# Kernel optimization log

Measured on AMD Instinct MI355X. Metric: run time of the kernel, lower is better.

## Reference

```python
import jax, jax.numpy as jnp
import numpy as np


def conv2d(x, w, b=None):
    # 3x3, stride 1, pad 1, NCHW/OIHW
    y = jax.lax.conv_general_dilated(x, w, (1, 1), ((1, 1), (1, 1)),
                                     dimension_numbers=('NCHW', 'OIHW', 'NCHW'))
    return y if b is None else y + b[None, :, None, None]


def maxpool3s2(x):
    # MaxPool2d(kernel_size=3, stride=2, padding=1)
    return jax.lax.reduce_window(x, -jnp.inf, jax.lax.max,
                                 (1, 1, 3, 3), (1, 1, 2, 2),
                                 ((0, 0), (0, 0), (1, 1), (1, 1)))


def up2(x):
    # F.interpolate(scale_factor=2, mode='bilinear', align_corners=False)
    N, C, H, W = x.shape
    return jax.image.resize(x, (N, C, 2 * H, 2 * W), method='bilinear')


def deform_conv2d(x, offset, w, dg):
    # mmcv-style DeformConv2d (no modulation, no bias), 3x3, pad 1, stride 1.
    # offset: (N, dg*2*9, H, W) -> (N, dg, 9, (y,x), H, W)
    N, Cin, H, W = x.shape
    Cout = w.shape[0]
    K, pad = 9, 1
    Cg = Cin // dg
    off = offset.reshape(N, dg, K, 2, H, W)
    ky, kx = jnp.meshgrid(jnp.arange(3), jnp.arange(3), indexing='ij')
    kdy = (ky.reshape(K) - pad).astype(x.dtype)
    kdx = (kx.reshape(K) - pad).astype(x.dtype)
    gy = jnp.arange(H, dtype=x.dtype)
    gx = jnp.arange(W, dtype=x.dtype)
    py = off[:, :, :, 0] + gy[None, None, None, :, None] + kdy[None, None, :, None, None]
    px = off[:, :, :, 1] + gx[None, None, None, None, :] + kdx[None, None, :, None, None]
    y0f = jnp.floor(py)
    x0f = jnp.floor(px)
    wy = (py - y0f).reshape(N, dg, 1, K * H * W)
    wx = (px - x0f).reshape(N, dg, 1, K * H * W)
    y0 = y0f.astype(jnp.int32)
    x0 = x0f.astype(jnp.int32)
    xg = x.reshape(N, dg, Cg, H * W)

    def gather(yi, xi):
        valid = ((yi >= 0) & (yi < H) & (xi >= 0) & (xi < W))
        idx = (jnp.clip(yi, 0, H - 1) * W + jnp.clip(xi, 0, W - 1)).reshape(N, dg, 1, K * H * W)
        v = jnp.take_along_axis(xg, idx, axis=-1)  # (N, dg, Cg, K*H*W)
        return v * valid.reshape(N, dg, 1, K * H * W).astype(x.dtype)

    v00 = gather(y0, x0)
    v01 = gather(y0, x0 + 1)
    v10 = gather(y0 + 1, x0)
    v11 = gather(y0 + 1, x0 + 1)
    col = (v00 * (1 - wy) * (1 - wx) + v01 * (1 - wy) * wx
           + v10 * wy * (1 - wx) + v11 * wy * wx)
    col = col.reshape(N, Cin, K, H, W)  # im2col with bilinear sampling
    return jnp.einsum('ock,nckhw->nohw', w.reshape(Cout, Cin, K), col)


def pyramid(img, blocks):
    feats = []
    x = img
    for w1, b1, w2, b2 in blocks:
        x = jax.nn.relu(conv2d(x, w1, b1))
        x = jax.nn.relu(conv2d(x, w2, b2))
        x = maxpool3s2(x)
        feats.append(x)
    return feats


def _forward(ref_image, unreg_image,
             fe0_w1, fe0_b1, fe0_w2, fe0_b2,
             fe1_w1, fe1_b1, fe1_w2, fe1_b2,
             fe2_w1, fe2_b1, fe2_w2, fe2_b2,
             ob0_w, ob0_b, ob1_w, ob1_b, ob2_w, ob2_b,
             og0_w, og0_b, og1_w, og1_b, og2_w, og2_b,
             dc0_w, dc1_w, dc2_w,
             fc0_w, fc0_b, fc1_w, fc1_b, fc2_w, fc2_b,
             dob_w, dob_b, dog_w, dog_b, ddc_w):
    relu = jax.nn.relu
    blocks = [(fe0_w1, fe0_b1, fe0_w2, fe0_b2),
              (fe1_w1, fe1_b1, fe1_w2, fe1_b2),
              (fe2_w1, fe2_b1, fe2_w2, fe2_b2)]
    rf = pyramid(ref_image, blocks)
    uf = pyramid(unreg_image, blocks)
    ob = [(ob0_w, ob0_b), (ob1_w, ob1_b), (ob2_w, ob2_b)]
    og = [(og0_w, og0_b), (og1_w, og1_b), (og2_w, og2_b)]
    dc = [dc0_w, dc1_w, dc2_w]
    fc = [(fc0_w, fc0_b), (fc1_w, fc1_b), (fc2_w, fc2_b)]
    offs = [None] * 3
    feats = [None] * 3
    for i in range(2, -1, -1):  # coarse to fine
        o = relu(conv2d(jnp.concatenate([rf[i], uf[i]], axis=1), *ob[i]))
        inp = o if i == 2 else jnp.concatenate([o, up2(offs[i + 1])], axis=1)
        offs[i] = relu(conv2d(inp, *og[i]))  # 18-channel offsets
        f = relu(deform_conv2d(uf[i], offs[i], dc[i], 1))
        finp = f if i == 2 else jnp.concatenate([f, up2(feats[i + 1])], axis=1)
        feats[i] = relu(conv2d(finp, *fc[i]))
    do = conv2d(jnp.concatenate([rf[0], feats[0]], axis=1), dob_w, dob_b)
    do = conv2d(jnp.concatenate([do, offs[0]], axis=1), dog_w, dog_b)  # 36-ch offsets
    return deform_conv2d(feats[0], do, ddc_w, 2)  # (N, 2, H/2, W/2)


def setup_inputs() -> dict:
    key = jax.random.key(0)
    ks = iter(jax.random.split(key, 48))
    IC = 16

    def W(cout, cin):
        return jax.random.normal(next(ks), (cout, cin, 3, 3), jnp.float32) / np.sqrt(cin * 9.0)

    def B(c):
        return jax.random.normal(next(ks), (c,), jnp.float32) * 0.01

    d = {
        'ref_image': jax.random.normal(next(ks), (4, 1, 512, 512), jnp.float32),
        'unreg_image': jax.random.normal(next(ks), (4, 1, 512, 512), jnp.float32),
        'fe0_w1': W(IC, 1), 'fe0_b1': B(IC), 'fe0_w2': W(IC, IC), 'fe0_b2': B(IC),
        'fe1_w1': W(IC, IC), 'fe1_b1': B(IC), 'fe1_w2': W(IC, IC), 'fe1_b2': B(IC),
        'fe2_w1': W(IC, IC), 'fe2_b1': B(IC), 'fe2_w2': W(IC, IC), 'fe2_b2': B(IC),
        'ob0_w': W(IC, 2 * IC), 'ob0_b': B(IC),
        'ob1_w': W(IC, 2 * IC), 'ob1_b': B(IC),
        'ob2_w': W(IC, 2 * IC), 'ob2_b': B(IC),
        'og0_w': W(18, IC + 18), 'og0_b': B(18),
        'og1_w': W(18, IC + 18), 'og1_b': B(18),
        'og2_w': W(18, IC), 'og2_b': B(18),
        'dc0_w': W(IC, IC), 'dc1_w': W(IC, IC), 'dc2_w': W(IC, IC),
        'fc0_w': W(IC, 2 * IC), 'fc0_b': B(IC),
        'fc1_w': W(IC, 2 * IC), 'fc1_b': B(IC),
        'fc2_w': W(IC, IC), 'fc2_b': B(IC),
        'dob_w': W(IC, 2 * IC), 'dob_b': B(IC),
        'dog_w': W(36, IC + 18), 'dog_b': B(36),
        'ddc_w': W(2, IC),
    }
    return d


def reference(ref_image, unreg_image,
              fe0_w1, fe0_b1, fe0_w2, fe0_b2,
              fe1_w1, fe1_b1, fe1_w2, fe1_b2,
              fe2_w1, fe2_b1, fe2_w2, fe2_b2,
              ob0_w, ob0_b, ob1_w, ob1_b, ob2_w, ob2_b,
              og0_w, og0_b, og1_w, og1_b, og2_w, og2_b,
              dc0_w, dc1_w, dc2_w,
              fc0_w, fc0_b, fc1_w, fc1_b, fc2_w, fc2_b,
              dob_w, dob_b, dog_w, dog_b, ddc_w):
    return _forward(ref_image, unreg_image,
                    fe0_w1, fe0_b1, fe0_w2, fe0_b2,
                    fe1_w1, fe1_b1, fe1_w2, fe1_b2,
                    fe2_w1, fe2_b1, fe2_w2, fe2_b2,
                    ob0_w, ob0_b, ob1_w, ob1_b, ob2_w, ob2_b,
                    og0_w, og0_b, og1_w, og1_b, og2_w, og2_b,
                    dc0_w, dc1_w, dc2_w,
                    fc0_w, fc0_b, fc1_w, fc1_b, fc2_w, fc2_b,
                    dob_w, dob_b, dog_w, dog_b, ddc_w)
```

## Files before the change

### kernel.cpp

```cpp
#include <hip/hip_runtime.h>
#include <math.h>

typedef _Float16 half2_t __attribute__((ext_vector_type(2)));
typedef _Float16 half8 __attribute__((ext_vector_type(8)));
typedef float floatx4 __attribute__((ext_vector_type(4)));

__device__ __forceinline__ unsigned packh2(float a, float b) {
  half2_t h;
  h.x = (_Float16)a;
  h.y = (_Float16)b;
  return __builtin_bit_cast(unsigned, h);
}
__device__ __forceinline__ unsigned short f2h(float a) {
  return __builtin_bit_cast(unsigned short, (_Float16)a);
}
__device__ __forceinline__ float h2f(unsigned short u) {
  return (float)__builtin_bit_cast(_Float16, u);
}

__global__ __launch_bounds__(256) void wreorder_k(
    const float* __restrict__ a, const float* __restrict__ b,
    const float* __restrict__ c, const float* __restrict__ d,
    float* __restrict__ out) {
  int t = blockIdx.x * 256 + threadIdx.x;
  if (t < 6912) {
    int which = t / 2304, r = t % 2304;
    int o = r % 16, kc = r / 16;
    int ci = kc % 16, k = kc / 16;
    const float* w = which == 0 ? a : (which == 1 ? b : c);
    out[t] = w[(o * 16 + ci) * 9 + k];
  } else if (t < 7200) {
    int r = t - 6912;
    int o = r % 2, kc = r / 2;
    int ci = kc % 16, k = kc / 16;
    out[t] = d[(o * 16 + ci) * 9 + k];
  }
}

__global__ __launch_bounds__(256) void wmfma_k(
    const float* __restrict__ w0, const float* __restrict__ w1,
    const float* __restrict__ w2, const float* __restrict__ w3,
    const float* __restrict__ w4, const float* __restrict__ w5,
    unsigned short* __restrict__ out) {
  int t = blockIdx.x * 256 + threadIdx.x;
  if (t >= 15360) return;
  int conv = t / 2560, r = t % 2560;
  int c = r / 512, L = (r / 8) % 64, j = r & 7;
  int quad = L >> 4, o = L & 15;
  int k = 32 * c + quad * 8 + j;
  int tap = k >> 4, cin = k & 15;
  float v;
  if (conv == 5) {
    v = (tap < 9 && cin == 0) ? w5[o * 9 + tap] : 0.f;
  } else {
    const float* w = conv == 0 ? w0 : conv == 1 ? w1 : conv == 2 ? w2 : conv == 3 ? w3 : w4;
    v = (tap < 9) ? w[((size_t)o * 16 + cin) * 9 + tap] : 0.f;
  }
  out[t] = f2h(v);
}

struct W32Entry { const float* src; int cin; };
struct W32Table { W32Entry e[8]; };
__global__ __launch_bounds__(256) void wmfma32_k(W32Table t, unsigned short* __restrict__ out) {
  int i = blockIdx.x * 256 + threadIdx.x;
  if (i >= 7 * 4608) return;
  int conv = i / 4608, r = i % 4608;
  int tap = r / 512, L = (r / 8) % 64, j = r & 7;
  int quad = L >> 4, o = L & 15;
  int c = quad * 8 + j;
  W32Entry en = t.e[conv];
  float v = (c < en.cin) ? en.src[((size_t)o * en.cin + c) * 9 + tap] : 0.f;
  out[i] = f2h(v);
}

struct SPEntry { const float* src; int cin; int cout; int ct; int dstoff; };
struct SPTable { SPEntry e[4]; };
__global__ __launch_bounds__(256) void wsplit_k(SPTable t, unsigned short* __restrict__ out) {
  SPEntry en = t.e[blockIdx.y];
  int aSize = en.ct * 2560;
  int bSize = (en.cin > 16) ? en.ct * 4608 : 0;
  int i = blockIdx.x * 256 + threadIdx.x;
  if (i >= aSize + bSize) return;
  float v;
  if (i < aSize) {
    int ct = i / 2560, r = i % 2560;
    int c = r / 512, L = (r / 8) % 64, j = r & 7;
    int quad = L >> 4, o16 = L & 15;
    int k = 32 * c + quad * 8 + j;
    int tap = k >> 4, cin = k & 15;
    int o = ct * 16 + o16;
    v = (tap < 9 && o < en.cout) ? en.src[((size_t)o * en.cin + cin) * 9 + tap] : 0.f;
  } else {
    int r2 = i - aSize;
    int ct = r2 / 4608, r = r2 % 4608;
    int tap = r / 512, L = (r / 8) % 64, j = r & 7;
    int quad = L >> 4, o16 = L & 15;
    int cin = quad * 8 + j;
    int o = ct * 16 + o16;
    v = (cin < en.cin - 16 && o < en.cout)
            ? en.src[((size_t)o * en.cin + 16 + cin) * 9 + tap] : 0.f;
  }
  out[en.dstoff + i] = f2h(v);
}

__device__ __forceinline__ void conv_mfma(
    const unsigned short* __restrict__ src, int SW,
    unsigned short* __restrict__ dst, int DPS, const half8* __restrict__ bf,
    const float* __restrict__ bias, int POS, int OW, int tid, int relu,
    int domask, int gby, int gbx, int bound) {
  const int lane = tid & 63, wid = tid >> 6;
  const int quad = lane >> 4, m = lane & 15;
  const int tap01 = quad >> 1, cin8 = (quad & 1) * 8;
  const int ntiles = (POS + 15) >> 4;
  float bs = bias[m];
  half8 zero;
#pragma unroll
  for (int j = 0; j < 8; ++j) zero[j] = (_Float16)0;
  for (int T = wid; T < ntiles; T += 4) {
    int pa = T * 16 + m;
    pa = pa < POS ? pa : POS - 1;
    int ya = pa / OW, xa = pa - ya * OW;
    floatx4 acc = {0.f, 0.f, 0.f, 0.f};
#pragma unroll
    for (int c = 0; c < 5; ++c) {
      int tap = 2 * c + tap01;
      half8 a = zero;
      if (tap < 9) {
        int dy = tap / 3, dx = tap - (tap / 3) * 3;
        a = *(const half8*)(src + ((ya + dy) * SW + xa + dx) * 16 + cin8);
      }
      acc = __builtin_amdgcn_mfma_f32_16x16x32_f16(a, bf[c], acc, 0, 0, 0);
    }
#pragma unroll
    for (int r = 0; r < 4; ++r) {
      int pd = T * 16 + quad * 4 + r;
      if (pd < POS) {
        float v = acc[r] + bs;
        if (relu) v = fmaxf(v, 0.f);
        if (domask) {
          int yd = pd / OW, xd = pd - (pd / OW) * OW;
          int gy = gby + yd, gx = gbx + xd;
          if (gy < 0 || gy >= bound || gx < 0 || gx >= bound) v = 0.f;
        }
        dst[pd * DPS + m] = f2h(v);
      }
    }
  }
}

__device__ __forceinline__ void conv_mfma32(
    const unsigned short* __restrict__ src, int SW,
    unsigned short* __restrict__ dst, int DPS, const half8* __restrict__ bf,
    const float* __restrict__ bias, int POS, int OW, int tid, int relu,
    int domask, int gby, int gbx, int bound) {
  const int lane = tid & 63, wid = tid >> 6;
  const int quad = lane >> 4, m = lane & 15;
  const int ntiles = (POS + 15) >> 4;
  float bs = bias[m];
  for (int T = wid; T < ntiles; T += 4) {
    int pa = T * 16 + m;
    pa = pa < POS ? pa : POS - 1;
    int ya = pa / OW, xa = pa - ya * OW;
    floatx4 acc = {0.f, 0.f, 0.f, 0.f};
#pragma unroll
    for (int tap = 0; tap < 9; ++tap) {
      int dy = tap / 3, dx = tap - (tap / 3) * 3;
      half8 a = *(const half8*)(src + ((ya + dy) * SW + xa + dx) * 32 + quad * 8);
      acc = __builtin_amdgcn_mfma_f32_16x16x32_f16(a, bf[tap], acc, 0, 0, 0);
    }
#pragma unroll
    for (int r = 0; r < 4; ++r) {
      int pd = T * 16 + quad * 4 + r;
      if (pd < POS) {
        float v = acc[r] + bs;
        if (relu) v = fmaxf(v, 0.f);
        if (domask) {
          int yd = pd / OW, xd = pd - (pd / OW) * OW;
          int gy = gby + yd, gx = gbx + xd;
          if (gy < 0 || gy >= bound || gx < 0 || gx >= bound) v = 0.f;
        }
        dst[pd * DPS + m] = f2h(v);
      }
    }
  }
}

template <int CT, int HASB, int NT>
__device__ __forceinline__ void conv_split_mfma(
    const unsigned short* __restrict__ srcB, const unsigned short* __restrict__ srcO,
    const unsigned short* __restrict__ wbase, float* __restrict__ outLds, int OSTRIDE,
    const float* __restrict__ bias, int NOUT, int relu, int tid) {
  const int lane = tid & 63, wid = tid >> 6;
  const int quad = lane >> 4, m = lane & 15;
  const int tap01 = quad >> 1, cin8 = (quad & 1) * 8;
  half8 zero;
#pragma unroll
  for (int j = 0; j < 8; ++j) zero[j] = (_Float16)0;
  floatx4 acc[CT][NT];
#pragma unroll
  for (int ct = 0; ct < CT; ++ct)
#pragma unroll
    for (int t = 0; t < NT; ++t) acc[ct][t] = floatx4{0.f, 0.f, 0.f, 0.f};
#pragma unroll
  for (int ct = 0; ct < CT; ++ct) {
    half8 bfA[5];
#pragma unroll
    for (int c = 0; c < 5; ++c)
      bfA[c] = *(const half8*)(wbase + ((ct * 5 + c) * 64 + lane) * 8);
#pragma unroll
    for (int t = 0; t < NT; ++t) {
      int pa = (wid + 4 * t) * 16 + m;
      int ya = pa >> 4, xa = pa & 15;
#pragma unroll
      for (int c = 0; c < 5; ++c) {
        int tap = 2 * c + tap01;
        half8 a = zero;
        if (tap < 9) {
          int dy = tap / 3, dx = tap - (tap / 3) * 3;
          a = *(const half8*)(srcB + ((ya + dy) * 18 + xa + dx) * 18 + cin8);
        }
        acc[ct][t] = __builtin_amdgcn_mfma_f32_16x16x32_f16(a, bfA[c], acc[ct][t], 0, 0, 0);
      }
    }
  }
  if (HASB) {
    const unsigned short* wb = wbase + CT * 2560;
#pragma unroll
    for (int ct = 0; ct < CT; ++ct) {
      half8 bfB[9];
#pragma unroll
      for (int c = 0; c < 9; ++c)
        bfB[c] = *(const half8*)(wb + ((ct * 9 + c) * 64 + lane) * 8);
#pragma unroll
      for (int t = 0; t < NT; ++t) {
        int pa = (wid + 4 * t) * 16 + m;
        int ya = pa >> 4, xa = pa & 15;
#pragma unroll
        for (int tap = 0; tap < 9; ++tap) {
          int dy = tap / 3, dx = tap - (tap / 3) * 3;
          half8 a = *(const half8*)(srcO + ((ya + dy) * 18 + xa + dx) * 34 + quad * 8);
          acc[ct][t] = __builtin_amdgcn_mfma_f32_16x16x32_f16(a, bfB[tap], acc[ct][t], 0, 0, 0);
        }
      }
    }
  }
  __syncthreads();
#pragma unroll
  for (int ct = 0; ct < CT; ++ct) {
    int o = ct * 16 + m;
#pragma unroll
    for (int t = 0; t < NT; ++t) {
#pragma unroll
      for (int r = 0; r < 4; ++r) {
        int pd = (wid + 4 * t) * 16 + quad * 4 + r;
        if (o < NOUT) {
          float v = acc[ct][t][r] + bias[o];
          if (relu) v = fmaxf(v, 0.f);
          outLds[pd * OSTRIDE + o] = v;
        }
      }
    }
  }
}

__global__ __launch_bounds__(256) void fe0_fused_k(
    const float* __restrict__ refI, const float* __restrict__ unrI,
    const unsigned short* __restrict__ wm1, const float* __restrict__ b1,
    const unsigned short* __restrict__ wm2, const float* __restrict__ b2,
    float* __restrict__ outR, float* __restrict__ outU, float* __restrict__ outUH) {
  __shared__ __attribute__((aligned(16))) unsigned short bufA[441 * 16];
  __shared__ __attribute__((aligned(16))) unsigned short c1h[361 * 16];
  const int z = blockIdx.z;
  const int im = z >> 2, n = z & 3;
  const float* img = (im ? unrI : refI) + (size_t)n * 512 * 512;
  float* outp = (im ? outU : outR) + (size_t)n * 16 * 256 * 256;
  const int py0 = blockIdx.y * 8, px0 = blockIdx.x * 8;
  const int tid = threadIdx.x;

  half8 bf1[5], bf2[5];
  {
    const int lane = tid & 63;
#pragma unroll
    for (int c = 0; c < 5; ++c) {
      bf1[c] = *(const half8*)(wm1 + (c * 64 + lane) * 8);
      bf2[c] = *(const half8*)(wm2 + (c * 64 + lane) * 8);
    }
  }

  {
    unsigned* s32 = (unsigned*)bufA;
    for (int i = tid; i < 441; i += 256) {
      int yi = i / 21, xi = i - yi * 21;
      int gy = 2 * py0 - 3 + yi, gx = 2 * px0 - 3 + xi;
      float v = 0.f;
      if (gy >= 0 && gy < 512 && gx >= 0 && gx < 512) v = img[gy * 512 + gx];
      uint4 q0 = {packh2(v, 0.f), 0u, 0u, 0u};
      uint4 q1 = {0u, 0u, 0u, 0u};
      *(uint4*)(s32 + i * 8) = q0;
      *(uint4*)(s32 + i * 8 + 4) = q1;
    }
  }
  __syncthreads();

  conv_mfma(bufA, 21, c1h, 16, bf1, b1, 361, 19, tid, 1, 1, 2 * py0 - 2, 2 * px0 - 2, 512);
  __syncthreads();
  conv_mfma(c1h, 19, bufA, 18, bf2, b2, 289, 17, tid, 1, 0, 0, 0, 0);
  __syncthreads();

  unsigned short* stage = c1h;
  for (int i = tid; i < 1024; i += 256) {
    int c = i & 15, r = i >> 4;
    int py = r >> 3, px = r & 7;
    unsigned short m = 0;
#pragma unroll
    for (int dy = 0; dy < 3; ++dy) {
      int gy = 2 * (py0 + py) - 1 + dy;
      if (gy < 0 || gy >= 512) continue;
#pragma unroll
      for (int dx = 0; dx < 3; ++dx) {
        int gx = 2 * (px0 + px) - 1 + dx;
        if (gx < 0 || gx >= 512) continue;
        unsigned short v = bufA[((2 * py + dy) * 17 + 2 * px + dx) * 18 + c];
        m = (v > m) ? v : m;
      }
    }
    stage[r * 18 + c] = m;
  }
  __syncthreads();

  for (int i = tid; i < 1024; i += 256) {
    int c = i >> 6, r = i & 63, py = r >> 3, px = r & 7;
    float mf = h2f(stage[r * 18 + c]);
    outp[((size_t)c * 256 + py0 + py) * 256 + px0 + px] = mf;
    if (im)
      outUH[(((size_t)n * 256 + py0 + py) * 256 + px0 + px) * 16 + c] = mf;
  }
}

__global__ __launch_bounds__(256) void fe12_fused_k(
    const float* __restrict__ in,
    const unsigned short* __restrict__ wm1, const float* __restrict__ b1,
    const unsigned short* __restrict__ wm2, const float* __restrict__ b2,
    float* __restrict__ outC, float* __restrict__ outHWC, int Hin) {
  __shared__ __attribute__((aligned(16))) unsigned short inh[441 * 16];
  __shared__ __attribute__((aligned(16))) unsigned short c1h[361 * 16];
  const int n = blockIdx.z;
  const int Ho = Hin >> 1;
  const int py0 = blockIdx.y * 8, px0 = blockIdx.x * 8;
  const int tid = threadIdx.x;
  const float* inN = in + (size_t)n * 16 * Hin * Hin;
  const size_t HH = (size_t)Hin * Hin;

  half8 bf1[5], bf2[5];
  {
    const int lane = tid & 63;
#pragma unroll
    for (int c = 0; c < 5; ++c) {
      bf1[c] = *(const half8*)(wm1 + (c * 64 + lane) * 8);
      bf2[c] = *(const half8*)(wm2 + (c * 64 + lane) * 8);
    }
  }

  unsigned* inh32 = (unsigned*)inh;
  for (int i = tid; i < 8 * 441; i += 256) {
    int cp = i / 441, r = i - cp * 441;
    int yi = r / 21, xi = r - yi * 21;
    int gy = 2 * py0 - 3 + yi, gx = 2 * px0 - 3 + xi;
    float v0 = 0.f, v1 = 0.f;
    if (gy >= 0 && gy < Hin && gx >= 0 && gx < Hin) {
      const float* s = inN + (size_t)(2 * cp) * HH + (size_t)gy * Hin + gx;
      v0 = s[0];
      v1 = s[HH];
    }
    inh32[r * 8 + cp] = packh2(v0, v1);
  }
  __syncthreads();

  conv_mfma(inh, 21, c1h, 16, bf1, b1, 361, 19, tid, 1, 1, 2 * py0 - 2, 2 * px0 - 2, Hin);
  __syncthreads();
  conv_mfma(c1h, 19, inh, 18, bf2, b2, 289, 17, tid, 1, 0, 0, 0, 0);
  __syncthreads();

  unsigned short* stage = c1h;
  for (int i = tid; i < 1024; i += 256) {
    int c = i & 15, r = i >> 4;
    int py = r >> 3, px = r & 7;
    unsigned short m = 0;
#pragma unroll
    for (int dy = 0; dy < 3; ++dy) {
      int gy = 2 * (py0 + py) - 1 + dy;
      if (gy < 0 || gy >= Hin) continue;
#pragma unroll
      for (int dx = 0; dx < 3; ++dx) {
        int gx = 2 * (px0 + px) - 1 + dx;
        if (gx < 0 || gx >= Hin) continue;
        unsigned short v = inh[((2 * py + dy) * 17 + 2 * px + dx) * 18 + c];
        m = (v > m) ? v : m;
      }
    }
    stage[r * 18 + c] = m;
  }
  __syncthreads();

  float* outp = outC + (size_t)n * 16 * Ho * Ho;
  for (int i = tid; i < 1024; i += 256) {
    int c = i >> 6, r = i & 63, py = r >> 3, px = r & 7;
    float mf = h2f(stage[r * 18 + c]);
    outp[((size_t)c * Ho + py0 + py) * Ho + px0 + px] = mf;
    if (n >= 4)
      outHWC[(((size_t)(n - 4) * Ho + py0 + py) * Ho + px0 + px) * 16 + c] = mf;
  }
}

template <int HAS_UP>
__global__ __launch_bounds__(256) void obog_k(
    const float* __restrict__ rf, const float* __restrict__ uf,
    const float* __restrict__ offsUp,
    const unsigned short* __restrict__ wmob, const float* __restrict__ bob,
    const unsigned short* __restrict__ wog, const float* __restrict__ bog,
    float* __restrict__ offsOut, int H) {
  __shared__ __attribute__((aligned(16))) unsigned POOL[5460];
  const int n = blockIdx.z;
  const int bx = blockIdx.x * 16, by = blockIdx.y * 8;
  const int tid = threadIdx.x;
  const size_t HH = (size_t)H * H;
  const float* r0 = rf + (size_t)n * 16 * HH;
  const float* u0 = uf + (size_t)n * 16 * HH;

  for (int i = tid; i < 3840; i += 256) {
    int cp = i / 240, r = i - cp * 240;
    int ly = r / 20, lx = r - ly * 20;
    int gy = by + ly - 2, gx = bx + lx - 2;
    float v0 = 0.f, v1 = 0.f;
    if (gy >= 0 && gy < H && gx >= 0 && gx < H) {
      const float* s = (cp < 8) ? r0 + (size_t)(2 * cp) * HH : u0 + (size_t)(2 * cp - 16) * HH;
      size_t off = (size_t)gy * H + gx;
      v0 = s[off];
      v1 = s[HH + off];
    }
    POOL[r * 16 + cp] = packh2(v0, v1);
  }
  __syncthreads();

  {
    half8 bf[9];
    const int lane = tid & 63;
#pragma unroll
    for (int c = 0; c < 9; ++c) bf[c] = *(const half8*)(wmob + (c * 64 + lane) * 8);
    conv_mfma32((const unsigned short*)POOL, 20, (unsigned short*)(POOL + 3840), 18,
                bf, bob, 180, 18, tid, 1, 1, by - 1, bx - 1, H);
  }
  __syncthreads();

  if (HAS_UP) {
    const int H2 = H >> 1;
    const float* os = offsUp + (size_t)n * 18 * H2 * H2;
    for (int i = tid; i < 16 * 180; i += 256) {
      int cp = i / 180, r = i - cp * 180;
      unsigned val = 0u;
      if (cp < 9) {
        int y1 = r / 18, x1 = r - y1 * 18;
        int gy = by + y1 - 1, gx = bx + x1 - 1;
        if (gy >= 0 && gy < H && gx >= 0 && gx < H) {
          float sy = 0.5f * gy - 0.25f, sx = 0.5f * gx - 0.25f;
          float y0f = floorf(sy), x0f = floorf(sx);
          float wy = sy - y0f, wx = sx - x0f;
          int y0 = (int)y0f, x0 = (int)x0f;
          int y0c = min(max(y0, 0), H2 - 1), y1c = min(max(y0 + 1, 0), H2 - 1);
          int x0c = min(max(x0, 0), H2 - 1), x1c = min(max(x0 + 1, 0), H2 - 1);
          const float* sp = os + (size_t)(2 * cp) * H2 * H2;
          float v0 = (1.f - wy) * ((1.f - wx) * sp[y0c * H2 + x0c] + wx * sp[y0c * H2 + x1c]) +
                     wy * ((1.f - wx) * sp[y1c * H2 + x0c] + wx * sp[y1c * H2 + x1c]);
          sp += (size_t)H2 * H2;
          float v1 = (1.f - wy) * ((1.f - wx) * sp[y0c * H2 + x0c] + wx * sp[y0c * H2 + x1c]) +
                     wy * ((1.f - wx) * sp[y1c * H2 + x0c] + wx * sp[y1c * H2 + x1c]);
          val = packh2(v0, v1);
        }
      }
      POOL[r * 17 + cp] = val;
    }
    __syncthreads();
  }

  conv_split_mfma<2, HAS_UP, 2>((const unsigned short*)(POOL + 3840),
                                (const unsigned short*)POOL, wog,
                                (float*)POOL, 19, bog, 18, 1, tid);
  __syncthreads();

  {
    int pix = tid & 127, half = tid >> 7;
    const float* of = (const float*)POOL + (size_t)pix * 19 + half * 9;
    int ty = pix >> 4, tx = pix & 15;
    float* op = offsOut + (size_t)n * 18 * HH + (size_t)(half * 9) * HH +
                (size_t)(by + ty) * H + (bx + tx);
#pragma unroll
    for (int o = 0; o < 9; ++o) op[(size_t)o * HH] = of[o];
  }
}

template <int HAS_UP>
__global__ __launch_bounds__(256) void defc_k(
    const float* __restrict__ ufHWC, const float* __restrict__ offs,
    const float* __restrict__ wdef, const float* __restrict__ featsUp,
    const unsigned short* __restrict__ wmfc, const float* __restrict__ bfc,
    float* __restrict__ featsOut, float* __restrict__ outHwc, int H) {
  __shared__ __attribute__((aligned(16))) unsigned ldsC[180 * 17];
  const int n = blockIdx.z;
  const int bx = blockIdx.x * 16, by = blockIdx.y * 8;
  const int tid = threadIdx.x;
  const size_t HH = (size_t)H * H;
  const float* inN = ufHWC + (size_t)n * HH * 16;
  const float* offN = offs + (size_t)n * 18 * HH;

  half8 bf[9];
  {
    const int lane = tid & 63;
#pragma unroll
    for (int c = 0; c < 9; ++c) bf[c] = *(const half8*)(wmfc + (c * 64 + lane) * 8);
  }

  for (int p = tid; p < 180; p += 256) {
    int y1 = p / 18, x1 = p - y1 * 18;
    int h = by + y1 - 1, w = bx + x1 - 1;
    bool valid = (h >= 0 && h < H && w >= 0 && w < H);
    float acc[16];
#pragma unroll
    for (int o = 0; o < 16; ++o) acc[o] = 0.f;
    if (valid) {
      size_t hw = (size_t)h * H + w;
#pragma unroll
      for (int k = 0; k < 9; ++k) {
        int ky = k / 3 - 1, kx = k % 3 - 1;
        float oy = offN[(size_t)(2 * k) * HH + hw];
        float ox = offN[(size_t)(2 * k + 1) * HH + hw];
        float py = (float)(h + ky) + oy;
        float px = (float)(w + kx) + ox;
        float y0f = floorf(py), x0f = floorf(px);
        float fy = py - y0f, fx = px - x0f;
        int y0 = (int)y0f, x0 = (int)x0f;
        bool vy0 = ((unsigned)y0 < (unsigned)H);
        bool vy1 = ((unsigned)(y0 + 1) < (unsigned)H);
        bool vx0 = ((unsigned)x0 < (unsigned)H);
        bool vx1 = ((unsigned)(x0 + 1) < (unsigned)H);
        int y0c = min(max(y0, 0), H - 1), y1c = min(max(y0 + 1, 0), H - 1);
        int x0c = min(max(x0, 0), H - 1), x1c = min(max(x0 + 1, 0), H - 1);
        float w00 = (vy0 && vx0) ? (1.f - fy) * (1.f - fx) : 0.f;
        float w01 = (vy0 && vx1) ? (1.f - fy) * fx : 0.f;
        float w10 = (vy1 && vx0) ? fy * (1.f - fx) : 0.f;
        float w11 = (vy1 && vx1) ? fy * fx : 0.f;
        const float* p00 = inN + ((size_t)y0c * H + x0c) * 16;
        const float* p01 = inN + ((size_t)y0c * H + x1c) * 16;
        const float* p10 = inN + ((size_t)y1c * H + x0c) * 16;
        const float* p11 = inN + ((size_t)y1c * H + x1c) * 16;
        const float* wk = wdef + (size_t)k * 256;
#pragma unroll
        for (int c4 = 0; c4 < 4; ++c4) {
          float4 a00 = *(const float4*)(p00 + c4 * 4);
          float4 a01 = *(const float4*)(p01 + c4 * 4);
          float4 a10 = *(const float4*)(p10 + c4 * 4);
          float4 a11 = *(const float4*)(p11 + c4 * 4);
          float v0 = w00 * a00.x + w01 * a01.x + w10 * a10.x + w11 * a11.x;
          float v1 = w00 * a00.y + w01 * a01.y + w10 * a10.y + w11 * a11.y;
          float v2 = w00 * a00.z + w01 * a01.z + w10 * a10.z + w11 * a11.z;
          float v3 = w00 * a00.w + w01 * a01.w + w10 * a10.w + w11 * a11.w;
#pragma unroll
          for (int o = 0; o < 16; ++o) {
            float t0 = fmaf(v0, wk[(c4 * 4 + 0) * 16 + o], acc[o]);
            t0 = fmaf(v1, wk[(c4 * 4 + 1) * 16 + o], t0);
            t0 = fmaf(v2, wk[(c4 * 4 + 2) * 16 + o], t0);
            acc[o] = fmaf(v3, wk[(c4 * 4 + 3) * 16 + o], t0);
          }
        }
      }
    }
#pragma unroll
    for (int cc = 0; cc < 8; ++cc) {
      float a0 = valid ? fmaxf(acc[2 * cc], 0.f) : 0.f;
      float a1 = valid ? fmaxf(acc[2 * cc + 1], 0.f) : 0.f;
      ldsC[p * 17 + cc] = packh2(a0, a1);
      if (!HAS_UP) ldsC[p * 17 + 8 + cc] = 0u;
    }
  }

  if (HAS_UP) {
    const int H2 = H >> 1;
    const float* fu = featsUp + (size_t)n * 16 * H2 * H2;
    for (int i = tid; i < 8 * 180; i += 256) {
      int cp = i / 180, r = i - cp * 180;
      int y1 = r / 18, x1 = r - y1 * 18;
      int gy = by + y1 - 1, gx = bx + x1 - 1;
      float v0 = 0.f, v1 = 0.f;
      if (gy >= 0 && gy < H && gx >= 0 && gx < H) {
        float sy = 0.5f * gy - 0.25f, sx = 0.5f * gx - 0.25f;
        float y0f = floorf(sy), x0f = floorf(sx);
        float wy = sy - y0f, wx = sx - x0f;
        int y0 = (int)y0f, x0 = (int)x0f;
        int y0c = min(max(y0, 0), H2 - 1), y1c = min(max(y0 + 1, 0), H2 - 1);
        int x0c = min(max(x0, 0), H2 - 1), x1c = min(max(x0 + 1, 0), H2 - 1);
        const float* sp = fu + (size_t)(2 * cp) * H2 * H2;
        v0 = (1.f - wy) * ((1.f - wx) * sp[y0c * H2 + x0c] + wx * sp[y0c * H2 + x1c]) +
             wy * ((1.f - wx) * sp[y1c * H2 + x0c] + wx * sp[y1c * H2 + x1c]);
        sp += (size_t)H2 * H2;
        v1 = (1.f - wy) * ((1.f - wx) * sp[y0c * H2 + x0c] + wx * sp[y0c * H2 + x1c]) +
             wy * ((1.f - wx) * sp[y1c * H2 + x0c] + wx * sp[y1c * H2 + x1c]);
      }
      ldsC[r * 17 + 8 + cp] = packh2(v0, v1);
    }
  }
  __syncthreads();

  {
    const int lane = tid & 63, wid = tid >> 6;
    const int quad = lane >> 4, m = lane & 15;
    const unsigned short* src = (const unsigned short*)ldsC;
    float bs = bfc[m];
    for (int T = wid; T < 8; T += 4) {
      int pa = T * 16 + m;
      int ya = pa >> 4, xa = pa & 15;
      floatx4 acc = {0.f, 0.f, 0.f, 0.f};
#pragma unroll
      for (int tap = 0; tap < 9; ++tap) {
        int dy = tap / 3, dx = tap - (tap / 3) * 3;
        half8 a = *(const half8*)(src + ((ya + dy) * 18 + xa + dx) * 34 + quad * 8);
        acc = __builtin_amdgcn_mfma_f32_16x16x32_f16(a, bf[tap], acc, 0, 0, 0);
      }
#pragma unroll
      for (int r = 0; r < 4; ++r) {
        int pd = T * 16 + quad * 4 + r;
        int yd = pd >> 4, xd = pd & 15;
        float v = fmaxf(acc[r] + bs, 0.f);
        if (featsOut)
          featsOut[(size_t)n * 16 * HH + (size_t)m * HH + (size_t)(by + yd) * H + bx + xd] = v;
        if (outHwc)
          outHwc[((size_t)n * HH + (size_t)(by + yd) * H + bx + xd) * 16 + m] = v;
      }
    }
  }
}

__global__ __launch_bounds__(256) void final_k(
    const float* __restrict__ rf0, const float* __restrict__ f0hwc,
    const float* __restrict__ offs0,
    const unsigned short* __restrict__ wmdob, const float* __restrict__ bdob,
    const unsigned short* __restrict__ wdog, const float* __restrict__ bdog,
    const float* __restrict__ wddc, float* __restrict__ out) {
  __shared__ __attribute__((aligned(16))) unsigned POOL[5460];
  const int H = 256;
  const size_t HH = 65536;
  const int n = blockIdx.z;
  const int bx = blockIdx.x * 16, by = blockIdx.y * 8;
  const int tid = threadIdx.x;
  const float* r0 = rf0 + (size_t)n * 16 * HH;
  const float* f0h = f0hwc + (size_t)n * HH * 16;

  for (int i = tid; i < 3840; i += 256) {
    int cp = i / 240, r = i - cp * 240;
    int ly = r / 20, lx = r - ly * 20;
    int gy = by + ly - 2, gx = bx + lx - 2;
    float v0 = 0.f, v1 = 0.f;
    if (gy >= 0 && gy < H && gx >= 0 && gx < H) {
      if (cp < 8) {
        const float* s = r0 + (size_t)(2 * cp) * HH + (size_t)gy * H + gx;
        v0 = s[0];
        v1 = s[HH];
      } else {
        const float* s = f0h + ((size_t)gy * H + gx) * 16 + (2 * cp - 16);
        v0 = s[0];
        v1 = s[1];
      }
    }
    POOL[r * 16 + cp] = packh2(v0, v1);
  }
  __syncthreads();

  {
    half8 bf[9];
    const int lane = tid & 63;
#pragma unroll
    for (int c = 0; c < 9; ++c) bf[c] = *(const half8*)(wmdob + (c * 64 + lane) * 8);
    conv_mfma32((const unsigned short*)POOL, 20, (unsigned short*)(POOL + 3840), 18,
                bf, bdob, 180, 18, tid, 0, 1, by - 1, bx - 1, H);
  }
  __syncthreads();

  {
    const float* os = offs0 + (size_t)n * 18 * HH;
    for (int i = tid; i < 16 * 180; i += 256) {
      int cp = i / 180, r = i - cp * 180;
      unsigned val = 0u;
      if (cp < 9) {
        int y1 = r / 18, x1 = r - y1 * 18;
        int gy = by + y1 - 1, gx = bx + x1 - 1;
        if (gy >= 0 && gy < H && gx >= 0 && gx < H) {
          const float* s = os + (size_t)(2 * cp) * HH + (size_t)gy * H + gx;
          val = packh2(s[0], s[HH]);
        }
      }
      POOL[r * 17 + cp] = val;
    }
    __syncthreads();
  }

  conv_split_mfma<3, 1, 2>((const unsigned short*)(POOL + 3840),
                           (const unsigned short*)POOL, wdog,
                           (float*)POOL, 37, bdog, 36, 0, tid);
  __syncthreads();

  {
    const int pix = tid & 127, g = tid >> 7;
    const int ty = pix >> 4, tx = pix & 15;
    const int h = by + ty, w = bx + tx;
    const float* a18 = (const float*)POOL + (size_t)pix * 37 + g * 18;
    float rr[2] = {0.f, 0.f};
#pragma unroll
    for (int k = 0; k < 9; ++k) {
      int ky = k / 3 - 1, kx = k % 3 - 1;
      float oy = a18[k * 2 + 0];
      float ox = a18[k * 2 + 1];
      float py = (float)(h + ky) + oy;
      float px = (float)(w + kx) + ox;
      float y0f = floorf(py), x0f = floorf(px);
      float fy = py - y0f, fx = px - x0f;
      int y0 = (int)y0f, x0 = (int)x0f;
      bool vy0 = ((unsigned)y0 < (unsigned)H);
      bool vy1 = ((unsigned)(y0 + 1) < (unsigned)H);
      bool vx0 = ((unsigned)x0 < (unsigned)H);
      bool vx1 = ((unsigned)(x0 + 1) < (unsigned)H);
      int y0c = min(max(y0, 0), H - 1), y1c = min(max(y0 + 1, 0), H - 1);
      int x0c = min(max(x0, 0), H - 1), x1c = min(max(x0 + 1, 0), H - 1);
      float w00 = (vy0 && vx0) ? (1.f - fy) * (1.f - fx) : 0.f;
      float w01 = (vy0 && vx1) ? (1.f - fy) * fx : 0.f;
      float w10 = (vy1 && vx0) ? fy * (1.f - fx) : 0.f;
      float w11 = (vy1 && vx1) ? fy * fx : 0.f;
      const float* p00 = f0h + ((size_t)y0c * H + x0c) * 16 + g * 8;
      const float* p01 = f0h + ((size_t)y0c * H + x1c) * 16 + g * 8;
      const float* p10 = f0h + ((size_t)y1c * H + x0c) * 16 + g * 8;
      const float* p11 = f0h + ((size_t)y1c * H + x1c) * 16 + g * 8;
      const float* wk = wddc + (size_t)(k * 16 + g * 8) * 2;
#pragma unroll
      for (int c4 = 0; c4 < 2; ++c4) {
        float4 a00 = *(const float4*)(p00 + c4 * 4);
        float4 a01 = *(const float4*)(p01 + c4 * 4);
        float4 a10 = *(const float4*)(p10 + c4 * 4);
        float4 a11 = *(const float4*)(p11 + c4 * 4);
        float v0 = w00 * a00.x + w01 * a01.x + w10 * a10.x + w11 * a11.x;
        float v1 = w00 * a00.y + w01 * a01.y + w10 * a10.y + w11 * a11.y;
        float v2 = w00 * a00.z + w01 * a01.z + w10 * a10.z + w11 * a11.z;
        float v3 = w00 * a00.w + w01 * a01.w + w10 * a10.w + w11 * a11.w;
#pragma unroll
        for (int o = 0; o < 2; ++o) {
          float t0 = fmaf(v0, wk[(c4 * 4 + 0) * 2 + o], rr[o]);
          t0 = fmaf(v1, wk[(c4 * 4 + 1) * 2 + o], t0);
          t0 = fmaf(v2, wk[(c4 * 4 + 2) * 2 + o], t0);
          rr[o] = fmaf(v3, wk[(c4 * 4 + 3) * 2 + o], t0);
        }
      }
    }
    float* part = (float*)POOL + 4736 + g * 256;
    part[pix * 2 + 0] = rr[0];
    part[pix * 2 + 1] = rr[1];
  }
  __syncthreads();

  if (tid < 128) {
    const float* p0 = (const float*)POOL + 4736;
    const float* p1 = p0 + 256;
    int ty = tid >> 4, tx = tid & 15;
    int h = by + ty, w = bx + tx;
    out[((size_t)n * 2 + 0) * HH + (size_t)h * H + w] = p0[tid * 2 + 0] + p1[tid * 2 + 0];
    out[((size_t)n * 2 + 1) * HH + (size_t)h * H + w] = p0[tid * 2 + 1] + p1[tid * 2 + 1];
  }
}

extern "C" void kernel_launch(void* const* d_in, const int* in_sizes, int n_in,
                              void* d_out, int out_size, void* d_ws, size_t ws_size,
                              hipStream_t stream) {
  auto F = [&](int i) { return (const float*)d_in[i]; };
  const float* ref = F(0);
  const float* unr = F(1);
  const float* few1[3] = {F(2), F(6), F(10)};
  const float* feb1[3] = {F(3), F(7), F(11)};
  const float* few2[3] = {F(4), F(8), F(12)};
  const float* feb2[3] = {F(5), F(9), F(13)};
  const float* obw[3] = {F(14), F(16), F(18)};
  const float* obb[3] = {F(15), F(17), F(19)};
  const float* ogw[3] = {F(20), F(22), F(24)};
  const float* ogb[3] = {F(21), F(23), F(25)};
  const float* dcw[3] = {F(26), F(27), F(28)};
  const float* fcw[3] = {F(29), F(31), F(33)};
  const float* fcb[3] = {F(30), F(32), F(34)};
  const float* dobw = F(35);
  const float* dobb = F(36);
  const float* dogw = F(37);
  const float* dogb = F(38);
  const float* ddcw = F(39);

  float* ws = (float*)d_ws;
  size_t p = 0;
  auto alloc = [&](size_t nf) { float* r = ws + p; p += nf; return r; };
  float* rf0 = alloc((size_t)4 * 16 * 65536);
  float* uf0 = alloc((size_t)4 * 16 * 65536);
  float* rf1 = alloc((size_t)4 * 16 * 16384);
  float* uf1 = alloc((size_t)4 * 16 * 16384);
  float* rf2 = alloc((size_t)4 * 16 * 4096);
  float* uf2 = alloc((size_t)4 * 16 * 4096);
  float* offs0 = alloc((size_t)4 * 18 * 65536);
  float* offs1 = alloc((size_t)4 * 18 * 16384);
  float* offs2 = alloc((size_t)4 * 18 * 4096);
  float* feats1 = alloc((size_t)4 * 16 * 16384);
  float* feats2 = alloc((size_t)4 * 16 * 4096);
  float* ufH0 = alloc((size_t)4 * 16 * 65536);
  float* ufH1 = alloc((size_t)4 * 16 * 16384);
  float* ufH2 = alloc((size_t)4 * 16 * 4096);
  float* fHwc = alloc((size_t)4 * 16 * 65536);
  float* wt = alloc(7200);
  float* wmf = alloc(7680);
  float* wm32f = alloc(16200);
  float* wspl = alloc(27648);
  if (p * sizeof(float) > ws_size) return;
  const float* wt_dc[3] = {wt, wt + 2304, wt + 4608};
  const float* wt_ddc = wt + 6912;
  unsigned short* wmh = (unsigned short*)wmf;
  unsigned short* wm32 = (unsigned short*)wm32f;
  unsigned short* wsp = (unsigned short*)wspl;

  W32Table T32;
  T32.e[0] = {obw[0], 32}; T32.e[1] = {obw[1], 32}; T32.e[2] = {obw[2], 32};
  T32.e[3] = {dobw, 32};   T32.e[4] = {fcw[0], 32}; T32.e[5] = {fcw[1], 32};
  T32.e[6] = {fcw[2], 16};
  auto o32 = [](int i) { return i * 4608; };

  SPTable TS;
  TS.e[0] = {ogw[0], 34, 18, 2, 0};
  TS.e[1] = {ogw[1], 34, 18, 2, 14336};
  TS.e[2] = {ogw[2], 16, 18, 2, 28672};
  TS.e[3] = {dogw, 34, 36, 3, 33792};
  const int o_og[3] = {0, 14336, 28672};
  const int o_dog = 33792;

  wreorder_k<<<29, 256, 0, stream>>>(dcw[0], dcw[1], dcw[2], ddcw, wt);
  wmfma_k<<<60, 256, 0, stream>>>(few2[0], few1[1], few2[1], few1[2], few2[2],
                                  few1[0], wmh);
  wmfma32_k<<<126, 256, 0, stream>>>(T32, wm32);
  wsplit_k<<<dim3(84, 4), 256, 0, stream>>>(TS, wsp);

  fe0_fused_k<<<dim3(32, 32, 8), 256, 0, stream>>>(
      ref, unr, wmh + 5 * 2560, feb1[0], wmh, feb2[0], rf0, uf0, ufH0);
  fe12_fused_k<<<dim3(16, 16, 8), 256, 0, stream>>>(
      rf0, wmh + 2560, feb1[1], wmh + 2 * 2560, feb2[1], rf1, ufH1, 256);
  fe12_fused_k<<<dim3(8, 8, 8), 256, 0, stream>>>(
      rf1, wmh + 3 * 2560, feb1[2], wmh + 4 * 2560, feb2[2], rf2, ufH2, 128);

  obog_k<0><<<dim3(4, 8, 4), 256, 0, stream>>>(
      rf2, uf2, nullptr, wm32 + o32(2), obb[2], wsp + o_og[2], ogb[2], offs2, 64);
  defc_k<0><<<dim3(4, 8, 4), 256, 0, stream>>>(
      ufH2, offs2, wt_dc[2], nullptr, wm32 + o32(6), fcb[2], feats2, nullptr, 64);
  obog_k<1><<<dim3(8, 16, 4), 256, 0, stream>>>(
      rf1, uf1, offs2, wm32 + o32(1), obb[1], wsp + o_og[1], ogb[1], offs1, 128);
  defc_k<1><<<dim3(8, 16, 4), 256, 0, stream>>>(
      ufH1, offs1, wt_dc[1], feats2, wm32 + o32(5), fcb[1], feats1, nullptr, 128);
  obog_k<1><<<dim3(16, 32, 4), 256, 0, stream>>>(
      rf0, uf0, offs1, wm32 + o32(0), obb[0], wsp + o_og[0], ogb[0], offs0, 256);
  defc_k<1><<<dim3(16, 32, 4), 256, 0, stream>>>(
      ufH0, offs0, wt_dc[0], feats1, wm32 + o32(4), fcb[0], nullptr, fHwc, 256);

  final_k<<<dim3(16, 32, 4), 256, 0, stream>>>(
      rf0, fHwc, offs0, wm32 + o32(3), dobb, wsp + o_dog, dogb, wt_ddc,
      (float*)d_out);
}
```

Measured before the change: 610.2 us.

## Store HWC gather buffers in fp16 and enlarge final kernel tile

Switches the channel-last feature buffers used by the deformable-conv gathers (ufH0-2 and fHwc) from fp32 to fp16, which halves the bytes each bilinear gather reads and the bytes written when producing them. The final kernel tile grows from 16x8 to 16x16 pixels, so each thread now handles one pixel and covers both offset groups. This removes the partial-sum LDS reduction and its extra barrier, and shrinks halo overhead per output. In exchange the kernel uses more LDS, which may lower occupancy, and the stored features lose precision. Values that were already rounded through fp16 in LDS are now stored that way directly.

```diff
diff --git a/kernel.cpp b/kernel.cpp
--- a/kernel.cpp
+++ b/kernel.cpp
@@ -267,7 +267,8 @@
     const float* __restrict__ refI, const float* __restrict__ unrI,
     const unsigned short* __restrict__ wm1, const float* __restrict__ b1,
     const unsigned short* __restrict__ wm2, const float* __restrict__ b2,
-    float* __restrict__ outR, float* __restrict__ outU, float* __restrict__ outUH) {
+    float* __restrict__ outR, float* __restrict__ outU,
+    unsigned short* __restrict__ outUH) {
   __shared__ __attribute__((aligned(16))) unsigned short bufA[441 * 16];
   __shared__ __attribute__((aligned(16))) unsigned short c1h[361 * 16];
   const int z = blockIdx.z;
@@ -330,10 +331,10 @@
 
   for (int i = tid; i < 1024; i += 256) {
     int c = i >> 6, r = i & 63, py = r >> 3, px = r & 7;
-    float mf = h2f(stage[r * 18 + c]);
-    outp[((size_t)c * 256 + py0 + py) * 256 + px0 + px] = mf;
+    unsigned short hb = stage[r * 18 + c];
+    outp[((size_t)c * 256 + py0 + py) * 256 + px0 + px] = h2f(hb);
     if (im)
-      outUH[(((size_t)n * 256 + py0 + py) * 256 + px0 + px) * 16 + c] = mf;
+      outUH[(((size_t)n * 256 + py0 + py) * 256 + px0 + px) * 16 + c] = hb;
   }
 }
 
@@ -341,7 +342,7 @@
     const float* __restrict__ in,
     const unsigned short* __restrict__ wm1, const float* __restrict__ b1,
     const unsigned short* __restrict__ wm2, const float* __restrict__ b2,
-    float* __restrict__ outC, float* __restrict__ outHWC, int Hin) {
+    float* __restrict__ outC, unsigned short* __restrict__ outHWC, int Hin) {
   __shared__ __attribute__((aligned(16))) unsigned short inh[441 * 16];
   __shared__ __attribute__((aligned(16))) unsigned short c1h[361 * 16];
   const int n = blockIdx.z;
@@ -405,10 +406,10 @@
   float* outp = outC + (size_t)n * 16 * Ho * Ho;
   for (int i = tid; i < 1024; i += 256) {
     int c = i >> 6, r = i & 63, py = r >> 3, px = r & 7;
-    float mf = h2f(stage[r * 18 + c]);
-    outp[((size_t)c * Ho + py0 + py) * Ho + px0 + px] = mf;
+    unsigned short hb = stage[r * 18 + c];
+    outp[((size_t)c * Ho + py0 + py) * Ho + px0 + px] = h2f(hb);
     if (n >= 4)
-      outHWC[(((size_t)(n - 4) * Ho + py0 + py) * Ho + px0 + px) * 16 + c] = mf;
+      outHWC[(((size_t)(n - 4) * Ho + py0 + py) * Ho + px0 + px) * 16 + c] = hb;
   }
 }
 
@@ -500,16 +501,16 @@
 
 template <int HAS_UP>
 __global__ __launch_bounds__(256) void defc_k(
-    const float* __restrict__ ufHWC, const float* __restrict__ offs,
+    const unsigned short* __restrict__ ufHWC, const float* __restrict__ offs,
     const float* __restrict__ wdef, const float* __restrict__ featsUp,
     const unsigned short* __restrict__ wmfc, const float* __restrict__ bfc,
-    float* __restrict__ featsOut, float* __restrict__ outHwc, int H) {
+    float* __restrict__ featsOut, unsigned short* __restrict__ outHwc, int H) {
   __shared__ __attribute__((aligned(16))) unsigned ldsC[180 * 17];
   const int n = blockIdx.z;
   const int bx = blockIdx.x * 16, by = blockIdx.y * 8;
   const int tid = threadIdx.x;
   const size_t HH = (size_t)H * H;
-  const float* inN = ufHWC + (size_t)n * HH * 16;
+  const unsigned short* inN = ufHWC + (size_t)n * HH * 16;
   const float* offN = offs + (size_t)n * 18 * HH;
 
   half8 bf[9];
@@ -548,27 +549,25 @@
         float w01 = (vy0 && vx1) ? (1.f - fy) * fx : 0.f;
         float w10 = (vy1 && vx0) ? fy * (1.f - fx) : 0.f;
         float w11 = (vy1 && vx1) ? fy * fx : 0.f;
-        const float* p00 = inN + ((size_t)y0c * H + x0c) * 16;
-        const float* p01 = inN + ((size_t)y0c * H + x1c) * 16;
-        const float* p10 = inN + ((size_t)y1c * H + x0c) * 16;
-        const float* p11 = inN + ((size_t)y1c * H + x1c) * 16;
+        const unsigned short* p00 = inN + ((size_t)y0c * H + x0c) * 16;
+        const unsigned short* p01 = inN + ((size_t)y0c * H + x1c) * 16;
+        const unsigned short* p10 = inN + ((size_t)y1c * H + x0c) * 16;
+        const unsigned short* p11 = inN + ((size_t)y1c * H + x1c) * 16;
         const float* wk = wdef + (size_t)k * 256;
 #pragma unroll
-        for (int c4 = 0; c4 < 4; ++c4) {
-          float4 a00 = *(const float4*)(p00 + c4 * 4);
-          float4 a01 = *(const float4*)(p01 + c4 * 4);
-          float4 a10 = *(const float4*)(p10 + c4 * 4);
-          float4 a11 = *(const float4*)(p11 + c4 * 4);
-          float v0 = w00 * a00.x + w01 * a01.x + w10 * a10.x + w11 * a11.x;
-          float v1 = w00 * a00.y + w01 * a01.y + w10 * a10.y + w11 * a11.y;
-          float v2 = w00 * a00.z + w01 * a01.z + w10 * a10.z + w11 * a11.z;
-          float v3 = w00 * a00.w + w01 * a01.w + w10 * a10.w + w11 * a11.w;
-#pragma unroll
-          for (int o = 0; o < 16; ++o) {
-            float t0 = fmaf(v0, wk[(c4 * 4 + 0) * 16 + o], acc[o]);
-            t0 = fmaf(v1, wk[(c4 * 4 + 1) * 16 + o], t0);
-            t0 = fmaf(v2, wk[(c4 * 4 + 2) * 16 + o], t0);
-            acc[o] = fmaf(v3, wk[(c4 * 4 + 3) * 16 + o], t0);
+        for (int c8 = 0; c8 < 2; ++c8) {
+          half8 a00 = *(const half8*)(p00 + c8 * 8);
+          half8 a01 = *(const half8*)(p01 + c8 * 8);
+          half8 a10 = *(const half8*)(p10 + c8 * 8);
+          half8 a11 = *(const half8*)(p11 + c8 * 8);
+          const float* wk8 = wk + c8 * 128;
+#pragma unroll
+          for (int j = 0; j < 8; ++j) {
+            float v = w00 * (float)a00[j] + w01 * (float)a01[j] +
+                      w10 * (float)a10[j] + w11 * (float)a11[j];
+#pragma unroll
+            for (int o = 0; o < 16; ++o)
+              acc[o] = fmaf(v, wk8[j * 16 + o], acc[o]);
           }
         }
       }
@@ -632,44 +631,41 @@
         if (featsOut)
           featsOut[(size_t)n * 16 * HH + (size_t)m * HH + (size_t)(by + yd) * H + bx + xd] = v;
         if (outHwc)
-          outHwc[((size_t)n * HH + (size_t)(by + yd) * H + bx + xd) * 16 + m] = v;
+          outHwc[((size_t)n * HH + (size_t)(by + yd) * H + bx + xd) * 16 + m] = f2h(v);
       }
     }
   }
 }
 
 __global__ __launch_bounds__(256) void final_k(
-    const float* __restrict__ rf0, const float* __restrict__ f0hwc,
+    const float* __restrict__ rf0, const unsigned short* __restrict__ f0hwc,
     const float* __restrict__ offs0,
     const unsigned short* __restrict__ wmdob, const float* __restrict__ bdob,
     const unsigned short* __restrict__ wdog, const float* __restrict__ bdog,
     const float* __restrict__ wddc, float* __restrict__ out) {
-  __shared__ __attribute__((aligned(16))) unsigned POOL[5460];
+  __shared__ __attribute__((aligned(16))) unsigned POOL[9472];
   const int H = 256;
   const size_t HH = 65536;
   const int n = blockIdx.z;
-  const int bx = blockIdx.x * 16, by = blockIdx.y * 8;
+  const int bx = blockIdx.x * 16, by = blockIdx.y * 16;
   const int tid = threadIdx.x;
   const float* r0 = rf0 + (size_t)n * 16 * HH;
-  const float* f0h = f0hwc + (size_t)n * HH * 16;
-
-  for (int i = tid; i < 3840; i += 256) {
-    int cp = i / 240, r = i - cp * 240;
+  const unsigned short* f0h = f0hwc + (size_t)n * HH * 16;
+
+  for (int i = tid; i < 6400; i += 256) {
+    int cp = i / 400, r = i - cp * 400;
     int ly = r / 20, lx = r - ly * 20;
     int gy = by + ly - 2, gx = bx + lx - 2;
-    float v0 = 0.f, v1 = 0.f;
+    unsigned val = 0u;
     if (gy >= 0 && gy < H && gx >= 0 && gx < H) {
       if (cp < 8) {
         const float* s = r0 + (size_t)(2 * cp) * HH + (size_t)gy * H + gx;
-        v0 = s[0];
-        v1 = s[HH];
+        val = packh2(s[0], s[HH]);
       } else {
-        const float* s = f0h + ((size_t)gy * H + gx) * 16 + (2 * cp - 16);
-        v0 = s[0];
-        v1 = s[1];
-      }
-    }
-    POOL[r * 16 + cp] = packh2(v0, v1);
+        val = *(const unsigned*)(f0h + ((size_t)gy * H + gx) * 16 + (2 * cp - 16));
+      }
+    }
+    POOL[r * 16 + cp] = val;
   }
   __syncthreads();
 
@@ -678,15 +674,15 @@
     const int lane = tid & 63;
 #pragma unroll
     for (int c = 0; c < 9; ++c) bf[c] = *(const half8*)(wmdob + (c * 64 + lane) * 8);
-    conv_mfma32((const unsigned short*)POOL, 20, (unsigned short*)(POOL + 3840), 18,
-                bf, bdob, 180, 18, tid, 0, 1, by - 1, bx - 1, H);
+    conv_mfma32((const unsigned short*)POOL, 20, (unsigned short*)(POOL + 6400), 18,
+                bf, bdob, 324, 18, tid, 0, 1, by - 1, bx - 1, H);
   }
   __syncthreads();
 
   {
     const float* os = offs0 + (size_t)n * 18 * HH;
-    for (int i = tid; i < 16 * 180; i += 256) {
-      int cp = i / 180, r = i - cp * 180;
+    for (int i = tid; i < 16 * 324; i += 256) {
+      int cp = i / 324, r = i - cp * 324;
       unsigned val = 0u;
       if (cp < 9) {
         int y1 = r / 18, x1 = r - y1 * 18;
@@ -701,74 +697,58 @@
     __syncthreads();
   }
 
-  conv_split_mfma<3, 1, 2>((const unsigned short*)(POOL + 3840),
+  conv_split_mfma<3, 1, 4>((const unsigned short*)(POOL + 6400),
                            (const unsigned short*)POOL, wdog,
                            (float*)POOL, 37, bdog, 36, 0, tid);
   __syncthreads();
 
   {
-    const int pix = tid & 127, g = tid >> 7;
-    const int ty = pix >> 4, tx = pix & 15;
+    const int ty = tid >> 4, tx = tid & 15;
     const int h = by + ty, w = bx + tx;
-    const float* a18 = (const float*)POOL + (size_t)pix * 37 + g * 18;
+    const float* a36 = (const float*)POOL + (size_t)tid * 37;
     float rr[2] = {0.f, 0.f};
 #pragma unroll
-    for (int k = 0; k < 9; ++k) {
-      int ky = k / 3 - 1, kx = k % 3 - 1;
-      float oy = a18[k * 2 + 0];
-      float ox = a18[k * 2 + 1];
-      float py = (float)(h + ky) + oy;
-      float px = (float)(w + kx) + ox;
-      float y0f = floorf(py), x0f = floorf(px);
-      float fy = py - y0f, fx = px - x0f;
-      int y0 = (int)y0f, x0 = (int)x0f;
-      bool vy0 = ((unsigned)y0 < (unsigned)H);
-      bool vy1 = ((unsigned)(y0 + 1) < (unsigned)H);
-      bool vx0 = ((unsigned)x0 < (unsigned)H);
-      bool vx1 = ((unsigned)(x0 + 1) < (unsigned)H);
-      int y0c = min(max(y0, 0), H - 1), y1c = min(max(y0 + 1, 0), H - 1);
-      int x0c = min(max(x0, 0), H - 1), x1c = min(max(x0 + 1, 0), H - 1);
-      float w00 = (vy0 && vx0) ? (1.f - fy) * (1.f - fx) : 0.f;
-      float w01 = (vy0 && vx1) ? (1.f - fy) * fx : 0.f;
-      float w10 = (vy1 && vx0) ? fy * (1.f - fx) : 0.f;
-      float w11 = (vy1 && vx1) ? fy * fx : 0.f;
-      const float* p00 = f0h + ((size_t)y0c * H + x0c) * 16 + g * 8;
-      const float* p01 = f0h + ((size_t)y0c * H + x1c) * 16 + g * 8;
-      const float* p10 = f0h + ((size_t)y1c * H + x0c) * 16 + g * 8;
-      const float* p11 = f0h + ((size_t)y1c * H + x1c) * 16 + g * 8;
-      const float* wk = wddc + (size_t)(k * 16 + g * 8) * 2;
-#pragma unroll
-      for (int c4 = 0; c4 < 2; ++c4) {
-        float4 a00 = *(const float4*)(p00 + c4 * 4);
-        float4 a01 = *(const float4*)(p01 + c4 * 4);
-        float4 a10 = *(const float4*)(p10 + c4 * 4);
-        float4 a11 = *(const float4*)(p11 + c4 * 4);
-        float v0 = w00 * a00.x + w01 * a01.x + w10 * a10.x + w11 * a11.x;
-        float v1 = w00 * a00.y + w01 * a01.y + w10 * a10.y + w11 * a11.y;
-        float v2 = w00 * a00.z + w01 * a01.z + w10 * a10.z + w11 * a11.z;
-        float v3 = w00 * a00.w + w01 * a01.w + w10 * a10.w + w11 * a11.w;
-#pragma unroll
-        for (int o = 0; o < 2; ++o) {
-          float t0 = fmaf(v0, wk[(c4 * 4 + 0) * 2 + o], rr[o]);
-          t0 = fmaf(v1, wk[(c4 * 4 + 1) * 2 + o], t0);
-          t0 = fmaf(v2, wk[(c4 * 4 + 2) * 2 + o], t0);
-          rr[o] = fmaf(v3, wk[(c4 * 4 + 3) * 2 + o], t0);
+    for (int g = 0; g < 2; ++g) {
+#pragma unroll
+      for (int k = 0; k < 9; ++k) {
+        int ky = k / 3 - 1, kx = k % 3 - 1;
+        float oy = a36[(g * 9 + k) * 2 + 0];
+        float ox = a36[(g * 9 + k) * 2 + 1];
+        float py = (float)(h + ky) + oy;
+        float px = (float)(w + kx) + ox;
+        float y0f = floorf(py), x0f = floorf(px);
+        float fy = py - y0f, fx = px - x0f;
+        int y0 = (int)y0f, x0 = (int)x0f;
+        bool vy0 = ((unsigned)y0 < (unsigned)H);
+        bool vy1 = ((unsigned)(y0 + 1) < (unsigned)H);
+        bool vx0 = ((unsigned)x0 < (unsigned)H);
+        bool vx1 = ((unsigned)(x0 + 1) < (unsigned)H);
+        int y0c = min(max(y0, 0), H - 1), y1c = min(max(y0 + 1, 0), H - 1);
+        int x0c = min(max(x0, 0), H - 1), x1c = min(max(x0 + 1, 0), H - 1);
+        float w00 = (vy0 && vx0) ? (1.f - fy) * (1.f - fx) : 0.f;
+        float w01 = (vy0 && vx1) ? (1.f - fy) * fx : 0.f;
+        float w10 = (vy1 && vx0) ? fy * (1.f - fx) : 0.f;
+        float w11 = (vy1 && vx1) ? fy * fx : 0.f;
+        const unsigned short* p00 = f0h + ((size_t)y0c * H + x0c) * 16 + g * 8;
+        const unsigned short* p01 = f0h + ((size_t)y0c * H + x1c) * 16 + g * 8;
+        const unsigned short* p10 = f0h + ((size_t)y1c * H + x0c) * 16 + g * 8;
+        const unsigned short* p11 = f0h + ((size_t)y1c * H + x1c) * 16 + g * 8;
+        half8 a00 = *(const half8*)p00;
+        half8 a01 = *(const half8*)p01;
+        half8 a10 = *(const half8*)p10;
+        half8 a11 = *(const half8*)p11;
+        const float* wk = wddc + (size_t)(k * 16 + g * 8) * 2;
+#pragma unroll
+        for (int j = 0; j < 8; ++j) {
+          float v = w00 * (float)a00[j] + w01 * (float)a01[j] +
+                    w10 * (float)a10[j] + w11 * (float)a11[j];
+          rr[0] = fmaf(v, wk[j * 2 + 0], rr[0]);
+          rr[1] = fmaf(v, wk[j * 2 + 1], rr[1]);
         }
       }
     }
-    float* part = (float*)POOL + 4736 + g * 256;
-    part[pix * 2 + 0] = rr[0];
-    part[pix * 2 + 1] = rr[1];
-  }
-  __syncthreads();
-
-  if (tid < 128) {
-    const float* p0 = (const float*)POOL + 4736;
-    const float* p1 = p0 + 256;
-    int ty = tid >> 4, tx = tid & 15;
-    int h = by + ty, w = bx + tx;
-    out[((size_t)n * 2 + 0) * HH + (size_t)h * H + w] = p0[tid * 2 + 0] + p1[tid * 2 + 0];
-    out[((size_t)n * 2 + 1) * HH + (size_t)h * H + w] = p0[tid * 2 + 1] + p1[tid * 2 + 1];
+    out[((size_t)n * 2 + 0) * HH + (size_t)h * H + w] = rr[0];
+    out[((size_t)n * 2 + 1) * HH + (size_t)h * H + w] = rr[1];
   }
 }
 
@@ -809,10 +789,10 @@
   float* offs2 = alloc((size_t)4 * 18 * 4096);
   float* feats1 = alloc((size_t)4 * 16 * 16384);
   float* feats2 = alloc((size_t)4 * 16 * 4096);
-  float* ufH0 = alloc((size_t)4 * 16 * 65536);
-  float* ufH1 = alloc((size_t)4 * 16 * 16384);
-  float* ufH2 = alloc((size_t)4 * 16 * 4096);
-  float* fHwc = alloc((size_t)4 * 16 * 65536);
+  unsigned short* ufH0 = (unsigned short*)alloc((size_t)4 * 16 * 65536 / 2);
+  unsigned short* ufH1 = (unsigned short*)alloc((size_t)4 * 16 * 16384 / 2);
+  unsigned short* ufH2 = (unsigned short*)alloc((size_t)4 * 16 * 4096 / 2);
+  unsigned short* fHwc = (unsigned short*)alloc((size_t)4 * 16 * 65536 / 2);
   float* wt = alloc(7200);
   float* wmf = alloc(7680);
   float* wm32f = alloc(16200);
@@ -864,7 +844,7 @@
   defc_k<1><<<dim3(16, 32, 4), 256, 0, stream>>>(
       ufH0, offs0, wt_dc[0], feats1, wm32 + o32(4), fcb[0], nullptr, fHwc, 256);
 
-  final_k<<<dim3(16, 32, 4), 256, 0, stream>>>(
+  final_k<<<dim3(16, 16, 4), 256, 0, stream>>>(
       rf0, fHwc, offs0, wm32 + o32(3), dobb, wsp + o_dog, dogb, wt_ddc,
       (float*)d_out);
 }
```

Measured after the change: 606.7 us. Within noise of the previous version (-0.6%).
